# Kernel optimization log

Hardware: AMD Instinct MI355X
Metric: run time of the kernel (lower is better)

The kernel has to match this reference:

```python
import jax, jax.numpy as jnp
import numpy as np

N = 16384
E = 262144
IN_F, HID, ENC = 3, 128, 768
NEG_SLOPE = 0.2
EPS = 1e-5


def _glorot(key, shape):
    lim = float(np.sqrt(6.0 / (shape[0] + shape[1])))
    return jax.random.uniform(key, shape, jnp.float32, -lim, lim)


def layernorm(x, g, b):
    mu = jnp.mean(x, axis=-1, keepdims=True)
    var = jnp.mean(jnp.square(x - mu), axis=-1, keepdims=True)
    return (x - mu) * jax.lax.rsqrt(var + EPS) * g + b


def gatv2(x, src, dst, Wl, bl, Wr, br, att, bias, n_nodes):
    # single-head GATv2: message = lin_l(x)[src], score from lin_l(x)[src] + lin_r(x)[dst]
    xl = x @ Wl + bl                                  # [N, C]
    xr = x @ Wr + br                                  # [N, C]
    e = jax.nn.leaky_relu(xl[src] + xr[dst], NEG_SLOPE) @ att   # [E]
    m = jax.ops.segment_max(e, dst, num_segments=n_nodes)       # per-dst max (self-loops => no empty segs)
    ex = jnp.exp(e - m[dst])
    denom = jax.ops.segment_sum(ex, dst, num_segments=n_nodes)
    alpha = ex / denom[dst]                           # [E]
    out = jax.ops.segment_sum(alpha[:, None] * xl[src], dst, num_segments=n_nodes)
    return out + bias


def setup_inputs() -> dict:
    key = jax.random.key(0)
    ks = jax.random.split(key, 12)
    x = jax.random.normal(ks[0], (N, IN_F), jnp.float32)
    edge_index = jax.random.randint(ks[1], (2, E), 0, N, jnp.int64)
    return {
        "x": x,
        "edge_index": edge_index,
        "Wfc": _glorot(ks[2], (IN_F, ENC)),
        "bfc": jnp.zeros((ENC,), jnp.float32),
        "W1l": _glorot(ks[3], (IN_F, HID)),
        "b1l": jnp.zeros((HID,), jnp.float32),
        "W1r": _glorot(ks[4], (IN_F, HID)),
        "b1r": jnp.zeros((HID,), jnp.float32),
        "att1": _glorot(ks[5], (HID, 1))[:, 0],
        "bias1": jnp.zeros((HID,), jnp.float32),
        "g_bn1": jnp.ones((HID,), jnp.float32),
        "bb_bn1": jnp.zeros((HID,), jnp.float32),
        "W2l": _glorot(ks[6], (HID, ENC)),
        "b2l": jnp.zeros((ENC,), jnp.float32),
        "W2r": _glorot(ks[7], (HID, ENC)),
        "b2r": jnp.zeros((ENC,), jnp.float32),
        "att2": _glorot(ks[8], (ENC, 1))[:, 0],
        "bias2": jnp.zeros((ENC,), jnp.float32),
        "g_norm": jnp.ones((ENC,), jnp.float32),
        "b_norm": jnp.zeros((ENC,), jnp.float32),
    }


def reference(x, edge_index, Wfc, bfc, W1l, b1l, W1r, b1r, att1, bias1,
              g_bn1, bb_bn1, W2l, b2l, W2r, b2r, att2, bias2, g_norm, b_norm):
    loops = jnp.arange(N, dtype=edge_index.dtype)
    src = jnp.concatenate([edge_index[0], loops])   # add self-loops (PyG default)
    dst = jnp.concatenate([edge_index[1], loops])
    res = x @ Wfc + bfc                              # [N, ENC]
    h = gatv2(x, src, dst, W1l, b1l, W1r, b1r, att1, bias1, N)
    h = jax.nn.elu(layernorm(h, g_bn1, bb_bn1))
    h = gatv2(h, src, dst, W2l, b2l, W2r, b2r, att2, bias2, N)
    return layernorm(h + res, g_norm, b_norm)
```

## Files before the change

### kernel.cpp

```cpp
#include <hip/hip_runtime.h>

#define N_NODES 16384
#define N_EDGES 262144
#define EP (N_EDGES + N_NODES)
#define HID 128
#define ENC 768
#define ENCP (ENC/2)
#define NEG 0.2f
#define EPSV 1e-5f

typedef unsigned short u16;
using f32x4  = __attribute__((ext_vector_type(4))) float;
using bf16x8 = __attribute__((ext_vector_type(8))) short;

__device__ __forceinline__ float wave_sum(float v){
  #pragma unroll
  for(int m=32;m>=1;m>>=1) v += __shfl_xor(v, m, 64);
  return v;
}
__device__ __forceinline__ float lrelu(float v){ return v > 0.f ? v : NEG*v; }
__device__ __forceinline__ unsigned bf16rtne(float f){
  const unsigned u = __float_as_uint(f);
  return (u + 0x7fffu + ((u>>16)&1u)) >> 16;
}
__device__ __forceinline__ unsigned pack2(float a, float b){
  return bf16rtne(a) | (bf16rtne(b) << 16);
}
__device__ __forceinline__ float bf2f(u16 h){ return __uint_as_float(((unsigned)h) << 16); }
__device__ __forceinline__ float plo(unsigned u){ return __uint_as_float(u << 16); }
__device__ __forceinline__ float phi(unsigned u){ return __uint_as_float(u & 0xffff0000u); }

__global__ __launch_bounds__(256) void lin1_kernel(
    const float* __restrict__ x,
    const float* __restrict__ Wl, const float* __restrict__ bl,
    const float* __restrict__ Wr, const float* __restrict__ br,
    unsigned* __restrict__ xl1p, unsigned* __restrict__ xr1p){
  const int i = blockIdx.x*256 + threadIdx.x;
  const int n = i >> 6, c = i & 63;
  const float x0 = x[n*3], x1 = x[n*3+1], x2 = x[n*3+2];
  const float la = x0*Wl[c]    + x1*Wl[HID+c]    + x2*Wl[2*HID+c]    + bl[c];
  const float lb = x0*Wl[c+64] + x1*Wl[HID+c+64] + x2*Wl[2*HID+c+64] + bl[c+64];
  const float ra = x0*Wr[c]    + x1*Wr[HID+c]    + x2*Wr[2*HID+c]    + br[c];
  const float rb = x0*Wr[c+64] + x1*Wr[HID+c+64] + x2*Wr[2*HID+c+64] + br[c+64];
  xl1p[i] = pack2(la, lb);
  xr1p[i] = pack2(ra, rb);
}

__global__ __launch_bounds__(256) void wprep_kernel(
    const float* __restrict__ W2l, const float* __restrict__ W2r,
    u16* __restrict__ Wtb){
  const int idx = blockIdx.x*256 + threadIdx.x;
  const int n = idx >> 7, k = idx & 127;
  const float v = (n < ENC) ? W2l[k*ENC + n] : W2r[k*ENC + (n-ENC)];
  Wtb[idx] = (u16)bf16rtne(v);
}

__global__ __launch_bounds__(256) void hist_kernel(
    const int* __restrict__ ei, int* __restrict__ hist){
  const int i = blockIdx.x*256 + threadIdx.x;
  const int dst = (i < N_EDGES) ? ei[N_EDGES + i] : (i - N_EDGES);
  atomicAdd(&hist[dst], 1);
}

__global__ __launch_bounds__(1024) void scan_kernel(
    const int* __restrict__ hist, int* __restrict__ rowstart){
  __shared__ int sums[1024];
  const int t = threadIdx.x;
  const int base = t*16;
  int loc[16];
  int s = 0;
  #pragma unroll
  for(int i=0;i<16;i++){ loc[i] = s; s += hist[base+i]; }
  sums[t] = s;
  __syncthreads();
  for(int off=1; off<1024; off<<=1){
    int v = 0;
    if(t >= off) v = sums[t-off];
    __syncthreads();
    if(t >= off) sums[t] += v;
    __syncthreads();
  }
  const int prev = (t==0) ? 0 : sums[t-1];
  #pragma unroll
  for(int i=0;i<16;i++) rowstart[base+i] = prev + loc[i];
  if(t == 1023) rowstart[N_NODES] = EP;
}

__global__ __launch_bounds__(256) void scatter_kernel(
    const int* __restrict__ ei, const int* __restrict__ rowstart,
    int* __restrict__ cursor, int* __restrict__ ssrc){
  const int i = blockIdx.x*256 + threadIdx.x;
  const int src = (i < N_EDGES) ? ei[i]           : (i - N_EDGES);
  const int dst = (i < N_EDGES) ? ei[N_EDGES + i] : (i - N_EDGES);
  const int pos = rowstart[dst] + atomicAdd(&cursor[dst], 1);
  ssrc[pos] = src;
}

__global__ __launch_bounds__(256) void node1_kernel(
    const unsigned* __restrict__ xl1p, const unsigned* __restrict__ xr1p,
    const float* __restrict__ att1, const float* __restrict__ bias1,
    const float* __restrict__ g1, const float* __restrict__ b1,
    const int* __restrict__ rowstart, const int* __restrict__ ssrc,
    u16* __restrict__ h1b, unsigned* __restrict__ h1p){
  const int lane = threadIdx.x & 63;
  const int n = blockIdx.x*4 + (threadIdx.x >> 6);
  const unsigned xru = xr1p[n*64 + lane];
  const float xra = plo(xru), xrb = phi(xru);
  const float aa = att1[lane], ab = att1[lane+64];
  float acc0 = 0.f, acc1 = 0.f, denom = 0.f;
  int p = rowstart[n];
  const int p1 = rowstart[n+1];
  for(; p+1 < p1; p += 2){
    const int s0 = ssrc[p], s1 = ssrc[p+1];
    const unsigned u0 = xl1p[s0*64 + lane];
    const unsigned u1 = xl1p[s1*64 + lane];
    const float a0 = plo(u0), b0 = phi(u0);
    const float a1 = plo(u1), b1v = phi(u1);
    float q0 = lrelu(a0+xra)*aa + lrelu(b0+xrb)*ab;
    float q1 = lrelu(a1+xra)*aa + lrelu(b1v+xrb)*ab;
    #pragma unroll
    for(int m=32;m>=1;m>>=1){
      q0 += __shfl_xor(q0, m, 64);
      q1 += __shfl_xor(q1, m, 64);
    }
    const float w0 = expf(q0), w1 = expf(q1);
    denom += w0 + w1;
    acc0 += w0*a0 + w1*a1;
    acc1 += w0*b0 + w1*b1v;
  }
  if(p < p1){
    const int s0 = ssrc[p];
    const unsigned u0 = xl1p[s0*64 + lane];
    const float a0 = plo(u0), b0 = phi(u0);
    const float e = wave_sum(lrelu(a0+xra)*aa + lrelu(b0+xrb)*ab);
    const float w0 = expf(e);
    denom += w0; acc0 += w0*a0; acc1 += w0*b0;
  }
  const float inv = 1.f/denom;
  const float y0 = acc0*inv + bias1[lane];
  const float y1 = acc1*inv + bias1[lane+64];
  const float mu  = wave_sum(y0+y1) * (1.f/HID);
  const float d0 = y0-mu, d1 = y1-mu;
  const float var = wave_sum(d0*d0 + d1*d1) * (1.f/HID);
  const float r = rsqrtf(var + EPSV);
  float z0 = d0*r*g1[lane] + b1[lane];
  float z1 = d1*r*g1[lane+64] + b1[lane+64];
  z0 = z0 > 0.f ? z0 : expm1f(z0);
  z1 = z1 > 0.f ? z1 : expm1f(z1);
  h1b[n*HID+lane]    = (u16)bf16rtne(z0);
  h1b[n*HID+lane+64] = (u16)bf16rtne(z1);
  h1p[n*64+lane]     = pack2(z0, z1);
}

#define LBM 128
#define LBN 128
__global__ __launch_bounds__(256) void mfma_lin2_kernel(
    const u16* __restrict__ h1b, const u16* __restrict__ Wtb,
    const float* __restrict__ b2l, const float* __restrict__ b2r,
    u16* __restrict__ xl2u, u16* __restrict__ xr2u){
  __shared__ __align__(16) u16 Cs[LBM*128];
  const int t = threadIdx.x;
  const int mb = blockIdx.x * LBM;
  const int nb = blockIdx.y * LBN;
  const int w = t >> 6, lane = t & 63;
  const int l15 = lane & 15, g = lane >> 4;
  const int ar0 = mb + w*32 + l15, ar1 = ar0 + 16;
  bf16x8 a0[4], a1[4];
  #pragma unroll
  for(int ks=0;ks<4;ks++){
    a0[ks] = *(const bf16x8*)(h1b + (size_t)ar0*128 + ks*32 + g*8);
    a1[ks] = *(const bf16x8*)(h1b + (size_t)ar1*128 + ks*32 + g*8);
  }
  f32x4 acc0[8], acc1[8];
  #pragma unroll
  for(int j=0;j<8;j++){ acc0[j]=(f32x4){0,0,0,0}; acc1[j]=(f32x4){0,0,0,0}; }
  #pragma unroll
  for(int j=0;j<8;j++){
    const int brn = nb + j*16 + l15;
    #pragma unroll
    for(int ks=0;ks<4;ks++){
      const bf16x8 b = *(const bf16x8*)(Wtb + (size_t)brn*128 + ks*32 + g*8);
      acc0[j] = __builtin_amdgcn_mfma_f32_16x16x32_bf16(a0[ks], b, acc0[j], 0,0,0);
      acc1[j] = __builtin_amdgcn_mfma_f32_16x16x32_bf16(a1[ks], b, acc1[j], 0,0,0);
    }
  }
  const float* bsrc = (nb < ENC) ? (b2l + nb) : (b2r + (nb - ENC));
  float biasj[8];
  #pragma unroll
  for(int j=0;j<8;j++) biasj[j] = bsrc[j*16 + l15];
  #pragma unroll
  for(int j=0;j<8;j++){
    const int coll = j*16 + l15;
    #pragma unroll
    for(int r4=0;r4<4;r4++){
      const int row0 = w*32 + g*4 + r4;
      *(u16*)((char*)Cs + row0*256 + ((coll*2) ^ ((row0&7)<<4))) =
          (u16)bf16rtne(acc0[j][r4] + biasj[j]);
      const int row1 = row0 + 16;
      *(u16*)((char*)Cs + row1*256 + ((coll*2) ^ ((row1&7)<<4))) =
          (u16)bf16rtne(acc1[j][r4] + biasj[j]);
    }
  }
  __syncthreads();
  u16* dst0 = (nb < ENC) ? (xl2u + nb) : (xr2u + (nb - ENC));
  const int rr = t >> 4, cc = t & 15;
  #pragma unroll
  for(int it=0; it<8; ++it){
    const int row = it*16 + rr;
    const uint4 v = *(const uint4*)((const char*)Cs + row*256 + ((cc*16) ^ ((row&7)<<4)));
    *(uint4*)(dst0 + (size_t)(mb+row)*ENC + cc*8) = v;
  }
}

__global__ __launch_bounds__(256) void node2b_kernel(
    const unsigned* __restrict__ xl2b, const unsigned* __restrict__ xr2b,
    const float* __restrict__ att2, const unsigned* __restrict__ h1p,
    const int* __restrict__ rowstart, const int* __restrict__ ssrc,
    u16* __restrict__ aggb){
  const int lane = threadIdx.x & 63;
  const int n = blockIdx.x*4 + (threadIdx.x >> 6);
  unsigned xrp[6]; float2 at[6];
  const unsigned* xrrow = xr2b + (size_t)n*ENCP;
  const float2* att22 = (const float2*)att2;
  #pragma unroll
  for(int j=0;j<6;j++){
    const int pidx = lane + 64*j;
    xrp[j] = xrrow[pidx]; at[j] = att22[pidx];
  }
  float denom = 0.f, acc0 = 0.f, acc1 = 0.f;
  int p = rowstart[n];
  const int p1 = rowstart[n+1];
  for(; p+1 < p1; p += 2){
    const int s0 = ssrc[p], s1 = ssrc[p+1];
    const unsigned* r0 = xl2b + (size_t)s0*ENCP;
    const unsigned* r1 = xl2b + (size_t)s1*ENCP;
    unsigned v0[6], v1[6];
    #pragma unroll
    for(int j=0;j<6;j++){ v0[j] = r0[lane + 64*j]; v1[j] = r1[lane + 64*j]; }
    const unsigned hu0 = h1p[s0*64 + lane];
    const unsigned hu1 = h1p[s1*64 + lane];
    float q0 = 0.f, q1 = 0.f;
    #pragma unroll
    for(int j=0;j<6;j++){
      q0 += lrelu(plo(v0[j])+plo(xrp[j]))*at[j].x + lrelu(phi(v0[j])+phi(xrp[j]))*at[j].y;
      q1 += lrelu(plo(v1[j])+plo(xrp[j]))*at[j].x + lrelu(phi(v1[j])+phi(xrp[j]))*at[j].y;
    }
    #pragma unroll
    for(int m=32;m>=1;m>>=1){
      q0 += __shfl_xor(q0, m, 64);
      q1 += __shfl_xor(q1, m, 64);
    }
    const float w0 = expf(q0), w1 = expf(q1);
    denom += w0 + w1;
    acc0 += w0*plo(hu0) + w1*plo(hu1);
    acc1 += w0*phi(hu0) + w1*phi(hu1);
  }
  if(p < p1){
    const int s0 = ssrc[p];
    const unsigned* r0 = xl2b + (size_t)s0*ENCP;
    unsigned v0[6];
    #pragma unroll
    for(int j=0;j<6;j++) v0[j] = r0[lane + 64*j];
    const unsigned hu0 = h1p[s0*64 + lane];
    float q0 = 0.f;
    #pragma unroll
    for(int j=0;j<6;j++)
      q0 += lrelu(plo(v0[j])+plo(xrp[j]))*at[j].x + lrelu(phi(v0[j])+phi(xrp[j]))*at[j].y;
    const float e = wave_sum(q0);
    const float w0 = expf(e);
    denom += w0; acc0 += w0*plo(hu0); acc1 += w0*phi(hu0);
  }
  const float inv = 1.f/denom;
  aggb[n*HID+lane]    = (u16)bf16rtne(acc0*inv);
  aggb[n*HID+lane+64] = (u16)bf16rtne(acc1*inv);
}

#define YSTR 770
__global__ __launch_bounds__(256) void gemm3_mfma_kernel(
    const u16* __restrict__ aggb, const u16* __restrict__ Wtb,
    const float* __restrict__ b2l, const float* __restrict__ bias2,
    const float* __restrict__ x, const float* __restrict__ Wfc,
    const float* __restrict__ bfc,
    const float* __restrict__ gn, const float* __restrict__ bn,
    float* __restrict__ out){
  __shared__ u16 Ys[64*YSTR];
  __shared__ float cbs[ENC];
  __shared__ float wfs[3][ENC];
  __shared__ float mus[64], rss[64];
  const int t = threadIdx.x;
  const int mb = blockIdx.x * 64;
  for(int c=t; c<ENC; c+=256){
    cbs[c] = b2l[c] + bias2[c] + bfc[c];
    wfs[0][c] = Wfc[c]; wfs[1][c] = Wfc[ENC+c]; wfs[2][c] = Wfc[2*ENC+c];
  }
  const int w = t >> 6, lane = t & 63;
  const int l15 = lane & 15, g = lane >> 4;
  const int ar = mb + w*16 + l15;
  bf16x8 a[4];
  #pragma unroll
  for(int ks=0;ks<4;ks++)
    a[ks] = *(const bf16x8*)(aggb + (size_t)ar*128 + ks*32 + g*8);
  float xv0[4], xv1[4], xv2[4];
  #pragma unroll
  for(int r4=0;r4<4;r4++){
    const int rrow = mb + w*16 + g*4 + r4;
    xv0[r4] = x[rrow*3]; xv1[r4] = x[rrow*3+1]; xv2[r4] = x[rrow*3+2];
  }
  float rs[4] = {0,0,0,0}, rq[4] = {0,0,0,0};
  __syncthreads();
  #pragma unroll
  for(int sub=0; sub<6; ++sub){
    const int nb = sub*128;
    f32x4 acc[8];
    #pragma unroll
    for(int j=0;j<8;j++) acc[j]=(f32x4){0,0,0,0};
    #pragma unroll
    for(int j=0;j<8;j++){
      const int brn = nb + j*16 + l15;
      #pragma unroll
      for(int ks=0;ks<4;ks++){
        const bf16x8 b = *(const bf16x8*)(Wtb + (size_t)brn*128 + ks*32 + g*8);
        acc[j] = __builtin_amdgcn_mfma_f32_16x16x32_bf16(a[ks], b, acc[j], 0,0,0);
      }
    }
    #pragma unroll
    for(int j=0;j<8;j++){
      const int col = nb + j*16 + l15;
      const float cb = cbs[col];
      const float w0 = wfs[0][col], w1 = wfs[1][col], w2 = wfs[2][col];
      #pragma unroll
      for(int r4=0;r4<4;r4++){
        const int lrow = w*16 + g*4 + r4;
        const float y = acc[j][r4] + cb + xv0[r4]*w0 + xv1[r4]*w1 + xv2[r4]*w2;
        rs[r4] += y; rq[r4] += y*y;
        Ys[lrow*YSTR + col] = (u16)bf16rtne(y);
      }
    }
  }
  #pragma unroll
  for(int m=8;m>=1;m>>=1){
    #pragma unroll
    for(int r4=0;r4<4;r4++){
      rs[r4] += __shfl_xor(rs[r4], m, 64);
      rq[r4] += __shfl_xor(rq[r4], m, 64);
    }
  }
  if(l15 == 0){
    #pragma unroll
    for(int r4=0;r4<4;r4++){
      const int lrow = w*16 + g*4 + r4;
      const float mu = rs[r4] * (1.f/ENC);
      const float var = rq[r4] * (1.f/ENC) - mu*mu;
      mus[lrow] = mu;
      rss[lrow] = rsqrtf(var + EPSV);
    }
  }
  __syncthreads();
  float gv[12], bv[12];
  #pragma unroll
  for(int j2=0;j2<12;j2++){ gv[j2] = gn[lane + j2*64]; bv[j2] = bn[lane + j2*64]; }
  for(int r=0; r<16; ++r){
    const int lrow = w*16 + r;
    const float mu = mus[lrow], rstd = rss[lrow];
    float* orow = out + (size_t)(mb+lrow)*ENC;
    #pragma unroll
    for(int j2=0;j2<12;j2++){
      const float y = bf2f(Ys[lrow*YSTR + lane + j2*64]);
      orow[lane + j2*64] = (y - mu)*rstd*gv[j2] + bv[j2];
    }
  }
}

extern "C" void kernel_launch(void* const* d_in, const int* in_sizes, int n_in,
                              void* d_out, int out_size, void* d_ws, size_t ws_size,
                              hipStream_t stream) {
  const float* x    = (const float*)d_in[0];
  const int*   ei   = (const int*)  d_in[1];
  const float* Wfc  = (const float*)d_in[2];
  const float* bfc  = (const float*)d_in[3];
  const float* W1l  = (const float*)d_in[4];
  const float* b1l  = (const float*)d_in[5];
  const float* W1r  = (const float*)d_in[6];
  const float* b1r  = (const float*)d_in[7];
  const float* att1 = (const float*)d_in[8];
  const float* bias1= (const float*)d_in[9];
  const float* g1   = (const float*)d_in[10];
  const float* bb1  = (const float*)d_in[11];
  const float* W2l  = (const float*)d_in[12];
  const float* b2l  = (const float*)d_in[13];
  const float* W2r  = (const float*)d_in[14];
  const float* b2r  = (const float*)d_in[15];
  const float* att2 = (const float*)d_in[16];
  const float* bias2= (const float*)d_in[17];
  const float* gn   = (const float*)d_in[18];
  const float* bn   = (const float*)d_in[19];
  float* out = (float*)d_out;

  char* w = (char*)d_ws;
  auto alloc = [&](size_t bytes){ void* p = (void*)w; w += (bytes + 255) & ~(size_t)255; return p; };
  int*      hist     = (int*)     alloc((size_t)N_NODES*4);
  int*      cursor   = (int*)     alloc((size_t)N_NODES*4);
  int*      rowstart = (int*)     alloc((size_t)(N_NODES+1)*4);
  int*      ssrc     = (int*)     alloc((size_t)EP*4);
  unsigned* xl1p     = (unsigned*)alloc((size_t)N_NODES*64*4);
  unsigned* xr1p     = (unsigned*)alloc((size_t)N_NODES*64*4);
  u16*      h1b      = (u16*)     alloc((size_t)N_NODES*HID*2);
  unsigned* h1p      = (unsigned*)alloc((size_t)N_NODES*64*4);
  u16*      aggb     = (u16*)     alloc((size_t)N_NODES*HID*2);
  unsigned* xl2b     = (unsigned*)alloc((size_t)N_NODES*ENCP*4);
  unsigned* xr2b     = (unsigned*)alloc((size_t)N_NODES*ENCP*4);
  u16*      Wtb      = (u16*)     alloc((size_t)2*ENC*HID*2);

  hipMemsetAsync(hist, 0, (size_t)N_NODES*8, stream);

  lin1_kernel<<<N_NODES*64/256, 256, 0, stream>>>(x, W1l, b1l, W1r, b1r, xl1p, xr1p);
  wprep_kernel<<<2*ENC*HID/256, 256, 0, stream>>>(W2l, W2r, Wtb);
  hist_kernel<<<EP/256, 256, 0, stream>>>(ei, hist);
  scan_kernel<<<1, 1024, 0, stream>>>(hist, rowstart);
  scatter_kernel<<<EP/256, 256, 0, stream>>>(ei, rowstart, cursor, ssrc);
  node1_kernel<<<N_NODES/4, 256, 0, stream>>>(xl1p, xr1p, att1, bias1, g1, bb1,
                                              rowstart, ssrc, h1b, h1p);
  mfma_lin2_kernel<<<dim3(N_NODES/LBM, 2*ENC/LBN), 256, 0, stream>>>(
      h1b, Wtb, b2l, b2r, (u16*)xl2b, (u16*)xr2b);
  node2b_kernel<<<N_NODES/4, 256, 0, stream>>>(xl2b, xr2b, att2, h1p,
                                               rowstart, ssrc, aggb);
  gemm3_mfma_kernel<<<N_NODES/64, 256, 0, stream>>>(aggb, Wtb, b2l, bias2,
                                                    x, Wfc, bfc, gn, bn, out);
}
```

Measured before the change: 223.1 us.

## Decompose leaky-ReLU attention into abs term plus precomputed per-node dots

Rewrites leaky_relu(v)·a as 0.6·v·a + 0.4·|v|·a. The linear part becomes per-node dot products (dotl/dotr), computed once in a fused prep kernel and in node1 via a precomputed W2·att2 vector, so each edge only evaluates an abs-weighted sum and adds two scalars. It also merges lin1, wprep and hist into one launch, vectorises the node2b loads to uint2, and switches to __expf. The risks are extra per-node scalar gathers and small numerical differences, because the linear term is now computed in fp32 from unrounded values.

```diff
diff --git a/kernel.cpp b/kernel.cpp
--- a/kernel.cpp
+++ b/kernel.cpp
@@ -6,7 +6,6 @@
 #define HID 128
 #define ENC 768
 #define ENCP (ENC/2)
-#define NEG 0.2f
 #define EPSV 1e-5f
 
 typedef unsigned short u16;
@@ -18,7 +17,6 @@
   for(int m=32;m>=1;m>>=1) v += __shfl_xor(v, m, 64);
   return v;
 }
-__device__ __forceinline__ float lrelu(float v){ return v > 0.f ? v : NEG*v; }
 __device__ __forceinline__ unsigned bf16rtne(float f){
   const unsigned u = __float_as_uint(f);
   return (u + 0x7fffu + ((u>>16)&1u)) >> 16;
@@ -30,36 +28,61 @@
 __device__ __forceinline__ float plo(unsigned u){ return __uint_as_float(u << 16); }
 __device__ __forceinline__ float phi(unsigned u){ return __uint_as_float(u & 0xffff0000u); }
 
-__global__ __launch_bounds__(256) void lin1_kernel(
+#define LIN1_BLKS (N_NODES/4)
+#define WPREP_BLKS (2*ENC*HID/256)
+#define HIST_BLKS (EP/256)
+#define W2A_BLKS 258
+__global__ __launch_bounds__(256) void prep_kernel(
     const float* __restrict__ x,
-    const float* __restrict__ Wl, const float* __restrict__ bl,
-    const float* __restrict__ Wr, const float* __restrict__ br,
-    unsigned* __restrict__ xl1p, unsigned* __restrict__ xr1p){
-  const int i = blockIdx.x*256 + threadIdx.x;
-  const int n = i >> 6, c = i & 63;
-  const float x0 = x[n*3], x1 = x[n*3+1], x2 = x[n*3+2];
-  const float la = x0*Wl[c]    + x1*Wl[HID+c]    + x2*Wl[2*HID+c]    + bl[c];
-  const float lb = x0*Wl[c+64] + x1*Wl[HID+c+64] + x2*Wl[2*HID+c+64] + bl[c+64];
-  const float ra = x0*Wr[c]    + x1*Wr[HID+c]    + x2*Wr[2*HID+c]    + br[c];
-  const float rb = x0*Wr[c+64] + x1*Wr[HID+c+64] + x2*Wr[2*HID+c+64] + br[c+64];
-  xl1p[i] = pack2(la, lb);
-  xr1p[i] = pack2(ra, rb);
-}
-
-__global__ __launch_bounds__(256) void wprep_kernel(
+    const float* __restrict__ W1l, const float* __restrict__ b1l,
+    const float* __restrict__ W1r, const float* __restrict__ b1r,
+    const float* __restrict__ att1,
     const float* __restrict__ W2l, const float* __restrict__ W2r,
-    u16* __restrict__ Wtb){
-  const int idx = blockIdx.x*256 + threadIdx.x;
-  const int n = idx >> 7, k = idx & 127;
-  const float v = (n < ENC) ? W2l[k*ENC + n] : W2r[k*ENC + (n-ENC)];
-  Wtb[idx] = (u16)bf16rtne(v);
-}
-
-__global__ __launch_bounds__(256) void hist_kernel(
-    const int* __restrict__ ei, int* __restrict__ hist){
-  const int i = blockIdx.x*256 + threadIdx.x;
-  const int dst = (i < N_EDGES) ? ei[N_EDGES + i] : (i - N_EDGES);
-  atomicAdd(&hist[dst], 1);
+    const float* __restrict__ b2l, const float* __restrict__ b2r,
+    const float* __restrict__ att2,
+    const int* __restrict__ ei,
+    unsigned* __restrict__ xl1p, unsigned* __restrict__ xr1p,
+    float* __restrict__ dotl1, float* __restrict__ dotr1,
+    u16* __restrict__ Wtb, float* __restrict__ w2a,
+    int* __restrict__ hist){
+  const int bid = blockIdx.x;
+  if(bid < LIN1_BLKS){
+    const int lane = threadIdx.x & 63;
+    const int n = bid*4 + (threadIdx.x >> 6);
+    const float x0 = x[n*3], x1 = x[n*3+1], x2 = x[n*3+2];
+    const int c0 = lane, c1 = lane + 64;
+    const float la = x0*W1l[c0] + x1*W1l[HID+c0] + x2*W1l[2*HID+c0] + b1l[c0];
+    const float lb = x0*W1l[c1] + x1*W1l[HID+c1] + x2*W1l[2*HID+c1] + b1l[c1];
+    const float ra = x0*W1r[c0] + x1*W1r[HID+c0] + x2*W1r[2*HID+c0] + b1r[c0];
+    const float rb = x0*W1r[c1] + x1*W1r[HID+c1] + x2*W1r[2*HID+c1] + b1r[c1];
+    const float aa = att1[c0], ab = att1[c1];
+    const float dl = wave_sum(la*aa + lb*ab);
+    const float dr = wave_sum(ra*aa + rb*ab);
+    if(lane == 0){ dotl1[n] = 0.6f*dl; dotr1[n] = 0.6f*dr; }
+    xl1p[n*64+lane] = pack2(la, lb);
+    xr1p[n*64+lane] = pack2(ra, rb);
+  } else if(bid < LIN1_BLKS + WPREP_BLKS){
+    const int idx = (bid - LIN1_BLKS)*256 + threadIdx.x;
+    const int n = idx >> 7, k = idx & 127;
+    const float v = (n < ENC) ? W2l[k*ENC + n] : W2r[k*ENC + (n-ENC)];
+    Wtb[idx] = (u16)bf16rtne(v);
+  } else if(bid < LIN1_BLKS + WPREP_BLKS + HIST_BLKS){
+    const int i = (bid - LIN1_BLKS - WPREP_BLKS)*256 + threadIdx.x;
+    const int dst = (i < N_EDGES) ? ei[N_EDGES + i] : (i - N_EDGES);
+    atomicAdd(&hist[dst], 1);
+  } else {
+    const int idx = bid - (LIN1_BLKS + WPREP_BLKS + HIST_BLKS);
+    const float* src = (idx < 128) ? (W2l + (size_t)idx*ENC)
+                     : (idx < 256) ? (W2r + (size_t)(idx-128)*ENC)
+                     : (idx == 256) ? b2l : b2r;
+    float partial = 0.f;
+    for(int c = threadIdx.x; c < ENC; c += 256) partial += src[c]*att2[c];
+    partial = wave_sum(partial);
+    __shared__ float red4[4];
+    if((threadIdx.x & 63) == 0) red4[threadIdx.x >> 6] = partial;
+    __syncthreads();
+    if(threadIdx.x == 0) w2a[idx] = red4[0]+red4[1]+red4[2]+red4[3];
+  }
 }
 
 __global__ __launch_bounds__(1024) void scan_kernel(
@@ -98,15 +121,20 @@
 
 __global__ __launch_bounds__(256) void node1_kernel(
     const unsigned* __restrict__ xl1p, const unsigned* __restrict__ xr1p,
-    const float* __restrict__ att1, const float* __restrict__ bias1,
+    const float* __restrict__ att1,
+    const float* __restrict__ dotl1, const float* __restrict__ dotr1,
+    const float* __restrict__ bias1,
     const float* __restrict__ g1, const float* __restrict__ b1,
+    const float* __restrict__ w2a,
     const int* __restrict__ rowstart, const int* __restrict__ ssrc,
-    u16* __restrict__ h1b, unsigned* __restrict__ h1p){
+    u16* __restrict__ h1b, unsigned* __restrict__ h1p,
+    float* __restrict__ dotl2, float* __restrict__ dotr2){
   const int lane = threadIdx.x & 63;
   const int n = blockIdx.x*4 + (threadIdx.x >> 6);
   const unsigned xru = xr1p[n*64 + lane];
   const float xra = plo(xru), xrb = phi(xru);
-  const float aa = att1[lane], ab = att1[lane+64];
+  const float sa = 0.4f*att1[lane], sb = 0.4f*att1[lane+64];
+  const float ebase = dotr1[n];
   float acc0 = 0.f, acc1 = 0.f, denom = 0.f;
   int p = rowstart[n];
   const int p1 = rowstart[n+1];
@@ -114,16 +142,17 @@
     const int s0 = ssrc[p], s1 = ssrc[p+1];
     const unsigned u0 = xl1p[s0*64 + lane];
     const unsigned u1 = xl1p[s1*64 + lane];
+    const float dl0 = dotl1[s0], dl1 = dotl1[s1];
     const float a0 = plo(u0), b0 = phi(u0);
     const float a1 = plo(u1), b1v = phi(u1);
-    float q0 = lrelu(a0+xra)*aa + lrelu(b0+xrb)*ab;
-    float q1 = lrelu(a1+xra)*aa + lrelu(b1v+xrb)*ab;
+    float q0 = fmaf(sa, __builtin_fabsf(a0+xra), sb*__builtin_fabsf(b0+xrb));
+    float q1 = fmaf(sa, __builtin_fabsf(a1+xra), sb*__builtin_fabsf(b1v+xrb));
     #pragma unroll
     for(int m=32;m>=1;m>>=1){
       q0 += __shfl_xor(q0, m, 64);
       q1 += __shfl_xor(q1, m, 64);
     }
-    const float w0 = expf(q0), w1 = expf(q1);
+    const float w0 = __expf(q0 + dl0 + ebase), w1 = __expf(q1 + dl1 + ebase);
     denom += w0 + w1;
     acc0 += w0*a0 + w1*a1;
     acc1 += w0*b0 + w1*b1v;
@@ -132,8 +161,8 @@
     const int s0 = ssrc[p];
     const unsigned u0 = xl1p[s0*64 + lane];
     const float a0 = plo(u0), b0 = phi(u0);
-    const float e = wave_sum(lrelu(a0+xra)*aa + lrelu(b0+xrb)*ab);
-    const float w0 = expf(e);
+    const float q = wave_sum(fmaf(sa, __builtin_fabsf(a0+xra), sb*__builtin_fabsf(b0+xrb)));
+    const float w0 = __expf(q + dotl1[s0] + ebase);
     denom += w0; acc0 += w0*a0; acc1 += w0*b0;
   }
   const float inv = 1.f/denom;
@@ -150,6 +179,17 @@
   h1b[n*HID+lane]    = (u16)bf16rtne(z0);
   h1b[n*HID+lane+64] = (u16)bf16rtne(z1);
   h1p[n*64+lane]     = pack2(z0, z1);
+  float dl2 = z0*w2a[lane]     + z1*w2a[lane+64];
+  float dr2 = z0*w2a[128+lane] + z1*w2a[128+lane+64];
+  #pragma unroll
+  for(int m=32;m>=1;m>>=1){
+    dl2 += __shfl_xor(dl2, m, 64);
+    dr2 += __shfl_xor(dr2, m, 64);
+  }
+  if(lane == 0){
+    dotl2[n] = 0.6f*(dl2 + w2a[256]);
+    dotr2[n] = 0.6f*(dr2 + w2a[257]);
+  }
 }
 
 #define LBM 128
@@ -214,60 +254,74 @@
 
 __global__ __launch_bounds__(256) void node2b_kernel(
     const unsigned* __restrict__ xl2b, const unsigned* __restrict__ xr2b,
-    const float* __restrict__ att2, const unsigned* __restrict__ h1p,
+    const float* __restrict__ att2,
+    const float* __restrict__ dotl2, const float* __restrict__ dotr2,
+    const unsigned* __restrict__ h1p,
     const int* __restrict__ rowstart, const int* __restrict__ ssrc,
     u16* __restrict__ aggb){
   const int lane = threadIdx.x & 63;
   const int n = blockIdx.x*4 + (threadIdx.x >> 6);
-  unsigned xrp[6]; float2 at[6];
-  const unsigned* xrrow = xr2b + (size_t)n*ENCP;
-  const float2* att22 = (const float2*)att2;
-  #pragma unroll
-  for(int j=0;j<6;j++){
-    const int pidx = lane + 64*j;
-    xrp[j] = xrrow[pidx]; at[j] = att22[pidx];
-  }
+  const uint2* xrrow = (const uint2*)(xr2b + (size_t)n*ENCP);
+  float xr[12], sg[12];
+  #pragma unroll
+  for(int k=0;k<3;k++){
+    const uint2 u = xrrow[lane + 64*k];
+    xr[4*k]   = plo(u.x); xr[4*k+1] = phi(u.x);
+    xr[4*k+2] = plo(u.y); xr[4*k+3] = phi(u.y);
+    const int cb = 4*(lane + 64*k);
+    sg[4*k]   = 0.4f*att2[cb];   sg[4*k+1] = 0.4f*att2[cb+1];
+    sg[4*k+2] = 0.4f*att2[cb+2]; sg[4*k+3] = 0.4f*att2[cb+3];
+  }
+  const float ebase = dotr2[n];
   float denom = 0.f, acc0 = 0.f, acc1 = 0.f;
   int p = rowstart[n];
   const int p1 = rowstart[n+1];
   for(; p+1 < p1; p += 2){
     const int s0 = ssrc[p], s1 = ssrc[p+1];
-    const unsigned* r0 = xl2b + (size_t)s0*ENCP;
-    const unsigned* r1 = xl2b + (size_t)s1*ENCP;
-    unsigned v0[6], v1[6];
-    #pragma unroll
-    for(int j=0;j<6;j++){ v0[j] = r0[lane + 64*j]; v1[j] = r1[lane + 64*j]; }
+    const uint2* r0 = (const uint2*)(xl2b + (size_t)s0*ENCP);
+    const uint2* r1 = (const uint2*)(xl2b + (size_t)s1*ENCP);
+    uint2 v0[3], v1[3];
+    #pragma unroll
+    for(int k=0;k<3;k++){ v0[k] = r0[lane + 64*k]; v1[k] = r1[lane + 64*k]; }
+    const float dl0 = dotl2[s0], dl1 = dotl2[s1];
     const unsigned hu0 = h1p[s0*64 + lane];
     const unsigned hu1 = h1p[s1*64 + lane];
     float q0 = 0.f, q1 = 0.f;
     #pragma unroll
-    for(int j=0;j<6;j++){
-      q0 += lrelu(plo(v0[j])+plo(xrp[j]))*at[j].x + lrelu(phi(v0[j])+phi(xrp[j]))*at[j].y;
-      q1 += lrelu(plo(v1[j])+plo(xrp[j]))*at[j].x + lrelu(phi(v1[j])+phi(xrp[j]))*at[j].y;
+    for(int k=0;k<3;k++){
+      q0 = fmaf(sg[4*k],   __builtin_fabsf(plo(v0[k].x)+xr[4*k]),   q0);
+      q0 = fmaf(sg[4*k+1], __builtin_fabsf(phi(v0[k].x)+xr[4*k+1]), q0);
+      q0 = fmaf(sg[4*k+2], __builtin_fabsf(plo(v0[k].y)+xr[4*k+2]), q0);
+      q0 = fmaf(sg[4*k+3], __builtin_fabsf(phi(v0[k].y)+xr[4*k+3]), q0);
+      q1 = fmaf(sg[4*k],   __builtin_fabsf(plo(v1[k].x)+xr[4*k]),   q1);
+      q1 = fmaf(sg[4*k+1], __builtin_fabsf(phi(v1[k].x)+xr[4*k+1]), q1);
+      q1 = fmaf(sg[4*k+2], __builtin_fabsf(plo(v1[k].y)+xr[4*k+2]), q1);
+      q1 = fmaf(sg[4*k+3], __builtin_fabsf(phi(v1[k].y)+xr[4*k+3]), q1);
     }
     #pragma unroll
     for(int m=32;m>=1;m>>=1){
       q0 += __shfl_xor(q0, m, 64);
       q1 += __shfl_xor(q1, m, 64);
     }
-    const float w0 = expf(q0), w1 = expf(q1);
+    const float w0 = __expf(q0 + dl0 + ebase), w1 = __expf(q1 + dl1 + ebase);
     denom += w0 + w1;
     acc0 += w0*plo(hu0) + w1*plo(hu1);
     acc1 += w0*phi(hu0) + w1*phi(hu1);
   }
   if(p < p1){
     const int s0 = ssrc[p];
-    const unsigned* r0 = xl2b + (size_t)s0*ENCP;
-    unsigned v0[6];
-    #pragma unroll
-    for(int j=0;j<6;j++) v0[j] = r0[lane + 64*j];
+    const uint2* r0 = (const uint2*)(xl2b + (size_t)s0*ENCP);
+    float q0 = 0.f;
+    #pragma unroll
+    for(int k=0;k<3;k++){
+      const uint2 v = r0[lane + 64*k];
+      q0 = fmaf(sg[4*k],   __builtin_fabsf(plo(v.x)+xr[4*k]),   q0);
+      q0 = fmaf(sg[4*k+1], __builtin_fabsf(phi(v.x)+xr[4*k+1]), q0);
+      q0 = fmaf(sg[4*k+2], __builtin_fabsf(plo(v.y)+xr[4*k+2]), q0);
+      q0 = fmaf(sg[4*k+3], __builtin_fabsf(phi(v.y)+xr[4*k+3]), q0);
+    }
     const unsigned hu0 = h1p[s0*64 + lane];
-    float q0 = 0.f;
-    #pragma unroll
-    for(int j=0;j<6;j++)
-      q0 += lrelu(plo(v0[j])+plo(xrp[j]))*at[j].x + lrelu(phi(v0[j])+phi(xrp[j]))*at[j].y;
-    const float e = wave_sum(q0);
-    const float w0 = expf(e);
+    const float w0 = __expf(wave_sum(q0) + dotl2[s0] + ebase);
     denom += w0; acc0 += w0*plo(hu0); acc1 += w0*phi(hu0);
   }
   const float inv = 1.f/denom;
@@ -404,26 +458,32 @@
   int*      ssrc     = (int*)     alloc((size_t)EP*4);
   unsigned* xl1p     = (unsigned*)alloc((size_t)N_NODES*64*4);
   unsigned* xr1p     = (unsigned*)alloc((size_t)N_NODES*64*4);
+  float*    dotl1    = (float*)   alloc((size_t)N_NODES*4);
+  float*    dotr1    = (float*)   alloc((size_t)N_NODES*4);
+  float*    dotl2    = (float*)   alloc((size_t)N_NODES*4);
+  float*    dotr2    = (float*)   alloc((size_t)N_NODES*4);
   u16*      h1b      = (u16*)     alloc((size_t)N_NODES*HID*2);
   unsigned* h1p      = (unsigned*)alloc((size_t)N_NODES*64*4);
   u16*      aggb     = (u16*)     alloc((size_t)N_NODES*HID*2);
   unsigned* xl2b     = (unsigned*)alloc((size_t)N_NODES*ENCP*4);
   unsigned* xr2b     = (unsigned*)alloc((size_t)N_NODES*ENCP*4);
   u16*      Wtb      = (u16*)     alloc((size_t)2*ENC*HID*2);
+  float*    w2a      = (float*)   alloc((size_t)W2A_BLKS*4);
 
   hipMemsetAsync(hist, 0, (size_t)N_NODES*8, stream);
 
-  lin1_kernel<<<N_NODES*64/256, 256, 0, stream>>>(x, W1l, b1l, W1r, b1r, xl1p, xr1p);
-  wprep_kernel<<<2*ENC*HID/256, 256, 0, stream>>>(W2l, W2r, Wtb);
-  hist_kernel<<<EP/256, 256, 0, stream>>>(ei, hist);
+  prep_kernel<<<LIN1_BLKS+WPREP_BLKS+HIST_BLKS+W2A_BLKS, 256, 0, stream>>>(
+      x, W1l, b1l, W1r, b1r, att1, W2l, W2r, b2l, b2r, att2, ei,
+      xl1p, xr1p, dotl1, dotr1, Wtb, w2a, hist);
   scan_kernel<<<1, 1024, 0, stream>>>(hist, rowstart);
   scatter_kernel<<<EP/256, 256, 0, stream>>>(ei, rowstart, cursor, ssrc);
-  node1_kernel<<<N_NODES/4, 256, 0, stream>>>(xl1p, xr1p, att1, bias1, g1, bb1,
-                                              rowstart, ssrc, h1b, h1p);
+  node1_kernel<<<N_NODES/4, 256, 0, stream>>>(xl1p, xr1p, att1, dotl1, dotr1,
+                                              bias1, g1, bb1, w2a,
+                                              rowstart, ssrc, h1b, h1p, dotl2, dotr2);
   mfma_lin2_kernel<<<dim3(N_NODES/LBM, 2*ENC/LBN), 256, 0, stream>>>(
       h1b, Wtb, b2l, b2r, (u16*)xl2b, (u16*)xr2b);
-  node2b_kernel<<<N_NODES/4, 256, 0, stream>>>(xl2b, xr2b, att2, h1p,
-                                               rowstart, ssrc, aggb);
+  node2b_kernel<<<N_NODES/4, 256, 0, stream>>>(xl2b, xr2b, att2, dotl2, dotr2,
+                                               h1p, rowstart, ssrc, aggb);
   gemm3_mfma_kernel<<<N_NODES/64, 256, 0, stream>>>(aggb, Wtb, b2l, bias2,
                                                     x, Wfc, bfc, gn, bn, out);
 }
```

After: 216.9 us. 1.03x faster.
